# Performance work log

Measured on AMD Instinct MI355X. Metric: run time of the kernel, lower is better.

## Reference

```python
import jax, jax.numpy as jnp
import numpy as np

DIM = 768
NUM_HEADS = 12
HEAD_DIM = DIM // NUM_HEADS
SCALE = HEAD_DIM ** -0.5


def setup_inputs() -> dict:
    key = jax.random.key(0)
    ks = jax.random.split(key, 4)
    x = jax.random.normal(ks[0], (8, 1024, DIM), dtype=jnp.float32)
    # nn.Linear stores weight as [out, in]; we keep that convention.
    w_qkv = jax.random.normal(ks[1], (3 * DIM, DIM), dtype=jnp.float32) * (DIM ** -0.5)
    w_proj = jax.random.normal(ks[2], (DIM, DIM), dtype=jnp.float32) * (DIM ** -0.5)
    b_proj = jax.random.normal(ks[3], (DIM,), dtype=jnp.float32) * 0.02
    return {"x": x, "w_qkv": w_qkv, "w_proj": w_proj, "b_proj": b_proj}


def reference(x, w_qkv, w_proj, b_proj):
    B, N, C = x.shape
    H, D = NUM_HEADS, HEAD_DIM
    # qkv: [B, N, 3C] -> [3, B, H, N, D]
    qkv = jnp.einsum('bnc,oc->bno', x, w_qkv)
    qkv = qkv.reshape(B, N, 3, H, D).transpose(2, 0, 3, 1, 4)
    q, k, v = qkv[0] * SCALE, qkv[1], qkv[2]
    # attention scores [B, H, N, N]
    attn = jnp.einsum('bhnd,bhmd->bhnm', q, k)
    attn = jax.nn.softmax(attn, axis=-1)
    # weighted values -> [B, N, C]
    out = jnp.einsum('bhnm,bhmd->bhnd', attn, v)
    out = out.transpose(0, 2, 1, 3).reshape(B, N, C)
    # output projection
    return jnp.einsum('bnc,oc->bno', out, w_proj) + b_proj
```

## Files before the change

kernel.cpp:

```cpp
#include <hip/hip_runtime.h>
#include <hip/hip_bf16.h>
#include <math.h>


typedef unsigned short u16;
typedef __attribute__((ext_vector_type(8))) short bf16x8;
typedef __attribute__((ext_vector_type(4))) float f32x4;
typedef __attribute__((ext_vector_type(4))) unsigned int u32x4;

#define MFMA_BF16(a, b, c) __builtin_amdgcn_mfma_f32_16x16x32_bf16((a), (b), (c), 0, 0, 0)

static __device__ __forceinline__ void gld_lds16(const void* g, void* l) {
  __builtin_amdgcn_global_load_lds(
      (__attribute__((address_space(1))) void*)(g),
      (__attribute__((address_space(3))) void*)(l), 16, 0, 0);
}

static __device__ __forceinline__ u16 f2bf(float f) {
  __hip_bfloat16 h = __float2bfloat16(f);
  return *(u16*)&h;
}

static __device__ __forceinline__ float fast_exp2(float x) {
#if __has_builtin(__builtin_amdgcn_exp2f)
  return __builtin_amdgcn_exp2f(x);
#else
  return exp2f(x);
#endif
}

__global__ __launch_bounds__(256) void convert_kernel(
    const float* __restrict__ src, u16* __restrict__ dst, int n)
{
  const int i = (blockIdx.x * 256 + threadIdx.x) * 4;
  if (i + 3 >= n) {
    for (int k = 0; k < 4 && i + k < n; ++k) {
      float f = src[i + k];
      if (!isfinite(f)) f = 0.f;
      dst[i + k] = f2bf(f);
    }
    return;
  }
  const float4 v = *(const float4*)(src + i);
  float f0 = v.x, f1 = v.y, f2 = v.z, f3 = v.w;
  if (!isfinite(f0)) f0 = 0.f;
  if (!isfinite(f1)) f1 = 0.f;
  if (!isfinite(f2)) f2 = 0.f;
  if (!isfinite(f3)) f3 = 0.f;
  ushort4 o;
  o.x = f2bf(f0); o.y = f2bf(f1); o.z = f2bf(f2); o.w = f2bf(f3);
  *(ushort4*)(dst + i) = o;
}

__device__ __forceinline__ void gemm_tile_768(
    const u16* __restrict__ A, const u16* __restrict__ B,
    int m0, int n0, u16* ldsA, u16* ldsB, f32x4 acc[4][4])
{
  const int tid  = threadIdx.x;
  const int lane = tid & 63;
  const int wave = tid >> 6;
  const int quad = lane >> 4;
  const int l16  = lane & 15;
  const int wm = wave >> 1, wn = wave & 1;

  const u16* gA[4]; const u16* gB[4]; int ldsoff[4];
#pragma unroll
  for (int it = 0; it < 4; ++it) {
    const int c   = it * 256 + tid;
    const int row = c >> 3;
    const int cc  = (c & 7) ^ (row & 7);
    gA[it] = A + (size_t)(m0 + row) * 768 + cc * 8;
    gB[it] = B + (size_t)(n0 + row) * 768 + cc * 8;
    ldsoff[it] = (it * 256 + wave * 64) * 8;
  }

  for (int kt = 0; kt < 12; ++kt) {
    __syncthreads();
#pragma unroll
    for (int it = 0; it < 4; ++it) {
      gld_lds16(gA[it] + kt * 64, ldsA + ldsoff[it]);
      gld_lds16(gB[it] + kt * 64, ldsB + ldsoff[it]);
    }
    __syncthreads();
#pragma unroll
    for (int kc = 0; kc < 2; ++kc) {
      bf16x8 av[4], bv[4];
#pragma unroll
      for (int i = 0; i < 4; ++i) {
        const int rowA = wm * 64 + i * 16 + l16;
        av[i] = *(const bf16x8*)(ldsA + rowA * 64 + (((kc * 4 + quad) ^ (rowA & 7)) * 8));
        const int rowB = wn * 64 + i * 16 + l16;
        bv[i] = *(const bf16x8*)(ldsB + rowB * 64 + (((kc * 4 + quad) ^ (rowB & 7)) * 8));
      }
#pragma unroll
      for (int i = 0; i < 4; ++i)
#pragma unroll
        for (int j = 0; j < 4; ++j)
          acc[i][j] = MFMA_BF16(av[i], bv[j], acc[i][j]);
    }
  }
}


__global__ __launch_bounds__(256, 2) void qkv_gemm_kernel(
    const u16* __restrict__ X, const u16* __restrict__ W,
    __hip_bfloat16* __restrict__ Qb, __hip_bfloat16* __restrict__ Kb,
    __hip_bfloat16* __restrict__ Vb)
{
  __shared__ alignas(16) u16 ldsA[128 * 64];
  __shared__ alignas(16) u16 ldsB[128 * 64];
  const int n0 = blockIdx.x * 128;
  const int m0 = blockIdx.y * 128;
  f32x4 acc[4][4];
  const f32x4 zero = {0.f, 0.f, 0.f, 0.f};
#pragma unroll
  for (int i = 0; i < 4; ++i)
#pragma unroll
    for (int j = 0; j < 4; ++j) acc[i][j] = zero;

  gemm_tile_768(X, W, m0, n0, ldsA, ldsB, acc);

  const int tid = threadIdx.x, lane = tid & 63, wave = tid >> 6;
  const int quad = lane >> 4, l16 = lane & 15;
  const int wm = wave >> 1, wn = wave & 1;
#pragma unroll
  for (int j = 0; j < 4; ++j) {
    const int o = n0 + wn * 64 + j * 16 + l16;
    const int which = (o >= 1536) ? 2 : ((o >= 768) ? 1 : 0);
    const int oc = o - which * 768;
    const int h = oc >> 6, d = oc & 63;
    __hip_bfloat16* dst = (which == 0) ? Qb : ((which == 1) ? Kb : Vb);
    const float sc = (which == 0) ? 0.180336880f : 1.0f;
#pragma unroll
    for (int i = 0; i < 4; ++i) {
#pragma unroll
      for (int r = 0; r < 4; ++r) {
        const int m = m0 + wm * 64 + i * 16 + quad * 4 + r;
        const int b = m >> 10, n = m & 1023;
        const size_t idx = (((size_t)(b * 12 + h)) * 1024 + n) * 64 + d;
        dst[idx] = __float2bfloat16(acc[i][j][r] * sc);
      }
    }
  }
}

__global__ __launch_bounds__(256, 2) void proj_gemm_kernel(
    const u16* __restrict__ A, const u16* __restrict__ W,
    const float* __restrict__ bias, float* __restrict__ out)
{
  __shared__ alignas(16) u16 ldsA[128 * 64];
  __shared__ alignas(16) u16 ldsB[128 * 64];
  const int n0 = blockIdx.x * 128;
  const int m0 = blockIdx.y * 128;
  f32x4 acc[4][4];
  const f32x4 zero = {0.f, 0.f, 0.f, 0.f};
#pragma unroll
  for (int i = 0; i < 4; ++i)
#pragma unroll
    for (int j = 0; j < 4; ++j) acc[i][j] = zero;

  gemm_tile_768(A, W, m0, n0, ldsA, ldsB, acc);

  const int tid = threadIdx.x, lane = tid & 63, wave = tid >> 6;
  const int quad = lane >> 4, l16 = lane & 15;
  const int wm = wave >> 1, wn = wave & 1;
#pragma unroll
  for (int j = 0; j < 4; ++j) {
    const int o = n0 + wn * 64 + j * 16 + l16;
    const float bv = bias[o];
#pragma unroll
    for (int i = 0; i < 4; ++i)
#pragma unroll
      for (int r = 0; r < 4; ++r) {
        const int m = m0 + wm * 64 + i * 16 + quad * 4 + r;
        out[(size_t)m * 768 + o] = acc[i][j][r] + bv;
      }
  }
}

__global__ __launch_bounds__(256) void vtrans_kernel(
    const u16* __restrict__ V, u16* __restrict__ Vt)
{
  __shared__ alignas(16) u16 t[64][72];
  const int bh = blockIdx.x, nb = blockIdx.y;
  const int tid = threadIdx.x;
  const u16* src = V + ((size_t)bh * 1024 + nb * 64) * 64;
#pragma unroll
  for (int it = 0; it < 2; ++it) {
    const int c = it * 256 + tid;
    const int r = c >> 3, cc = c & 7;
    *(u32x4*)&t[r][cc * 8] = *(const u32x4*)(src + r * 64 + cc * 8);
  }
  __syncthreads();
  u16* dstbase = Vt + (size_t)bh * 64 * 1024 + nb * 64;
#pragma unroll
  for (int it = 0; it < 2; ++it) {
    const int c = it * 256 + tid;
    const int d = c >> 3, nc = c & 7;
    u32x4 o;
#pragma unroll
    for (int p = 0; p < 4; ++p) {
      const unsigned lo = t[nc * 8 + p * 2 + 0][d];
      const unsigned hi = t[nc * 8 + p * 2 + 1][d];
      o[p] = lo | (hi << 16);
    }
    *(u32x4*)(dstbase + (size_t)d * 1024 + nc * 8) = o;
  }
}

__global__ __launch_bounds__(256, 3) void attn_kernel(
    const u16* __restrict__ Q, const u16* __restrict__ K,
    const u16* __restrict__ Vt, __hip_bfloat16* __restrict__ O)
{
  __shared__ alignas(16) u16 ldsK[64 * 64];
  __shared__ alignas(16) u16 ldsV[64 * 64];
  __shared__ alignas(16) u16 pbuf[4 * 32 * 72];
  const int bh = blockIdx.x;
  const int qb = blockIdx.y;
  const int tid = threadIdx.x;
  const int wave = tid >> 6, lane = tid & 63;
  const int quad = lane >> 4, l16 = lane & 15;
  u16* pw = pbuf + wave * (32 * 72);

  const int q0 = qb * 128 + wave * 32;
  const u16* Kbh = K  + (size_t)bh * (1024 * 64);
  const u16* Vbh = Vt + (size_t)bh * (64 * 1024);

  const int c0   = tid;
  const int row0 = c0 >> 3,          slot0 = c0 & 7;
  const int row1 = (c0 + 256) >> 3,  slot1 = c0 & 7;
  const int cc0 = slot0 ^ (row0 & 7), cc1 = slot1 ^ (row1 & 7);
  const u16* gK0 = Kbh + (size_t)row0 * 64 + cc0 * 8;
  const u16* gK1 = Kbh + (size_t)row1 * 64 + cc1 * 8;
  const u16* gV0 = Vbh + (size_t)row0 * 1024 + cc0 * 8;
  const u16* gV1 = Vbh + (size_t)row1 * 1024 + cc1 * 8;
  const int ldso0 = (wave * 64) * 8, ldso1 = (256 + wave * 64) * 8;

  bf16x8 aQ0[2], aQ1[2];
#pragma unroll
  for (int s = 0; s < 2; ++s) {
    const u16* qp = Q + ((size_t)bh * 1024 + q0 + s * 16 + l16) * 64 + quad * 8;
    aQ0[s] = *(const bf16x8*)qp;
    aQ1[s] = *(const bf16x8*)(qp + 32);
  }

  f32x4 oacc[2][4];
  const f32x4 zero = {0.f, 0.f, 0.f, 0.f};
#pragma unroll
  for (int s = 0; s < 2; ++s)
#pragma unroll
    for (int db = 0; db < 4; ++db) oacc[s][db] = zero;
  float lacc[2][4] = {{0.f, 0.f, 0.f, 0.f}, {0.f, 0.f, 0.f, 0.f}};

  for (int kt = 0; kt < 16; ++kt) {
    __syncthreads();
    gld_lds16(gK0 + (size_t)kt * 64 * 64, ldsK + ldso0);
    gld_lds16(gK1 + (size_t)kt * 64 * 64, ldsK + ldso1);
    gld_lds16(gV0 + kt * 64, ldsV + ldso0);
    gld_lds16(gV1 + kt * 64, ldsV + ldso1);
    __syncthreads();

    bf16x8 kb0[4], kb1[4];
#pragma unroll
    for (int t = 0; t < 4; ++t) {
      const int row = t * 16 + l16;
      kb0[t] = *(const bf16x8*)(ldsK + row * 64 + (((0 * 4 + quad) ^ (row & 7)) * 8));
      kb1[t] = *(const bf16x8*)(ldsK + row * 64 + (((1 * 4 + quad) ^ (row & 7)) * 8));
    }
#pragma unroll
    for (int s = 0; s < 2; ++s) {
#pragma unroll
      for (int t = 0; t < 4; ++t) {
        f32x4 z = zero;
        z = MFMA_BF16(aQ0[s], kb0[t], z);
        z = MFMA_BF16(aQ1[s], kb1[t], z);
#pragma unroll
        for (int r = 0; r < 4; ++r) {
          const float p = fast_exp2(z[r]);
          lacc[s][r] += p;
          pw[(s * 16 + quad * 4 + r) * 72 + t * 16 + l16] = f2bf(p);
        }
      }
    }
    asm volatile("" ::: "memory");
    bf16x8 pa0[2], pa1[2];
#pragma unroll
    for (int s = 0; s < 2; ++s) {
      const u16* pb = pw + (s * 16 + l16) * 72 + quad * 8;
      pa0[s] = *(const bf16x8*)pb;
      pa1[s] = *(const bf16x8*)(pb + 32);
    }
#pragma unroll
    for (int db = 0; db < 4; ++db) {
      const int row = db * 16 + l16;
      const bf16x8 v0 = *(const bf16x8*)(ldsV + row * 64 + (((0 * 4 + quad) ^ (row & 7)) * 8));
      const bf16x8 v1 = *(const bf16x8*)(ldsV + row * 64 + (((1 * 4 + quad) ^ (row & 7)) * 8));
#pragma unroll
      for (int s = 0; s < 2; ++s) {
        oacc[s][db] = MFMA_BF16(pa0[s], v0, oacc[s][db]);
        oacc[s][db] = MFMA_BF16(pa1[s], v1, oacc[s][db]);
      }
    }
  }

  const int b = bh / 12, h = bh - (bh / 12) * 12;
#pragma unroll
  for (int s = 0; s < 2; ++s) {
#pragma unroll
    for (int r = 0; r < 4; ++r) {
      float lsum = lacc[s][r];
      lsum += __shfl_xor(lsum, 1);
      lsum += __shfl_xor(lsum, 2);
      lsum += __shfl_xor(lsum, 4);
      lsum += __shfl_xor(lsum, 8);
      const float inv = 1.f / lsum;
      const int n = q0 + s * 16 + quad * 4 + r;
      __hip_bfloat16* orow = O + ((size_t)b * 1024 + n) * 768 + h * 64;
#pragma unroll
      for (int db = 0; db < 4; ++db)
        orow[db * 16 + l16] = __float2bfloat16(oacc[s][db][r] * inv);
    }
  }
}

extern "C" void kernel_launch(void* const* d_in, const int* in_sizes, int n_in,
                              void* d_out, int out_size, void* d_ws, size_t ws_size,
                              hipStream_t stream) {
  const float* x      = (const float*)d_in[0];
  const float* w_qkv  = (const float*)d_in[1];
  const float* w_proj = (const float*)d_in[2];
  const float* b_proj = (const float*)d_in[3];
  float* out = (float*)d_out;

  char* ws = (char*)d_ws;
  const size_t SEG = (size_t)96 * 1024 * 64 * sizeof(u16);
  u16* xb   = (u16*)(ws + 0 * SEG);
  u16* Qb   = (u16*)(ws + 1 * SEG);
  u16* Kb   = (u16*)(ws + 2 * SEG);
  u16* Vb   = (u16*)(ws + 3 * SEG);
  u16* Vt   = (u16*)(ws + 4 * SEG);
  u16* wqb  = (u16*)(ws + 5 * SEG);
  u16* wpb  = (u16*)(ws + 5 * SEG + 3538944);
  u16* AO   = Vb;

  const int nx = 8 * 1024 * 768, nq = 2304 * 768, np = 768 * 768;
  convert_kernel<<<nx / 1024, 256, 0, stream>>>(x, xb, nx);
  convert_kernel<<<nq / 1024, 256, 0, stream>>>(w_qkv, wqb, nq);
  convert_kernel<<<np / 1024, 256, 0, stream>>>(w_proj, wpb, np);

  qkv_gemm_kernel<<<dim3(18, 64), 256, 0, stream>>>(
      xb, wqb, (__hip_bfloat16*)Qb, (__hip_bfloat16*)Kb, (__hip_bfloat16*)Vb);
  vtrans_kernel  <<<dim3(96, 16), 256, 0, stream>>>(Vb, Vt);
  attn_kernel    <<<dim3(96, 8), 256, 0, stream>>>(Qb, Kb, Vt, (__hip_bfloat16*)AO);
  proj_gemm_kernel<<<dim3(6, 64), 256, 0, stream>>>(AO, wpb, b_proj, out);
}
```

Measured before the change: 203.3 us.

## Fuse V transpose into QKV GEMM epilogue via LDS staging; merge weight conversions

The QKV GEMM epilogue now stages the output tile in LDS with a swizzled layout and writes Q/K rows and the transposed V directly using 16-byte vector stores. This removes the separate V-transpose kernel, its global round trip, and the scattered 2-byte stores of the old epilogue. The two weight conversions are also merged into one launch, and the scalar tail path in the converter is dropped. In exchange the epilogue adds two barriers and reuses the GEMM's shared memory.

Result: faster. 194.4 us (-4.4%).

```diff
diff --git a/kernel.cpp b/kernel.cpp
--- a/kernel.cpp
+++ b/kernel.cpp
@@ -29,18 +29,7 @@
 #endif
 }
 
-__global__ __launch_bounds__(256) void convert_kernel(
-    const float* __restrict__ src, u16* __restrict__ dst, int n)
-{
-  const int i = (blockIdx.x * 256 + threadIdx.x) * 4;
-  if (i + 3 >= n) {
-    for (int k = 0; k < 4 && i + k < n; ++k) {
-      float f = src[i + k];
-      if (!isfinite(f)) f = 0.f;
-      dst[i + k] = f2bf(f);
-    }
-    return;
-  }
+static __device__ __forceinline__ void conv4(const float* src, u16* dst, int i) {
   const float4 v = *(const float4*)(src + i);
   float f0 = v.x, f1 = v.y, f2 = v.z, f3 = v.w;
   if (!isfinite(f0)) f0 = 0.f;
@@ -52,6 +41,25 @@
   *(ushort4*)(dst + i) = o;
 }
 
+__global__ __launch_bounds__(256) void convert_kernel(
+    const float* __restrict__ src, u16* __restrict__ dst, int n)
+{
+  const int i = (blockIdx.x * 256 + threadIdx.x) * 4;
+  if (i < n) conv4(src, dst, i);
+}
+
+__global__ __launch_bounds__(256) void convert2_kernel(
+    const float* __restrict__ a, u16* __restrict__ da, int na_blk,
+    const float* __restrict__ b, u16* __restrict__ db)
+{
+  const int blk = blockIdx.x;
+  if (blk < na_blk) {
+    conv4(a, da, (blk * 256 + threadIdx.x) * 4);
+  } else {
+    conv4(b, db, ((blk - na_blk) * 256 + threadIdx.x) * 4);
+  }
+}
+
 __device__ __forceinline__ void gemm_tile_768(
     const u16* __restrict__ A, const u16* __restrict__ B,
     int m0, int n0, u16* ldsA, u16* ldsB, f32x4 acc[4][4])
@@ -104,8 +112,71 @@
 
 __global__ __launch_bounds__(256, 2) void qkv_gemm_kernel(
     const u16* __restrict__ X, const u16* __restrict__ W,
-    __hip_bfloat16* __restrict__ Qb, __hip_bfloat16* __restrict__ Kb,
-    __hip_bfloat16* __restrict__ Vb)
+    u16* __restrict__ Qb, u16* __restrict__ Kb, u16* __restrict__ Vt)
+{
+  __shared__ alignas(16) u16 lds[2 * 128 * 64];
+  u16* ldsA = lds;
+  u16* ldsB = lds + 128 * 64;
+  const int n0 = blockIdx.x * 128;
+  const int m0 = blockIdx.y * 128;
+  f32x4 acc[4][4];
+  const f32x4 zero = {0.f, 0.f, 0.f, 0.f};
+#pragma unroll
+  for (int i = 0; i < 4; ++i)
+#pragma unroll
+    for (int j = 0; j < 4; ++j) acc[i][j] = zero;
+
+  gemm_tile_768(X, W, m0, n0, ldsA, ldsB, acc);
+
+  const int tid = threadIdx.x, lane = tid & 63, wave = tid >> 6;
+  const int quad = lane >> 4, l16 = lane & 15;
+  const int wm = wave >> 1, wn = wave & 1;
+
+  const int which = blockIdx.x / 6;
+  const bool isV = (which == 2);
+  const float sc = (which == 0) ? 0.180336880f : 1.0f;
+  u16* ep = lds;
+
+  __syncthreads();
+#pragma unroll
+  for (int i = 0; i < 4; ++i)
+#pragma unroll
+    for (int j = 0; j < 4; ++j)
+#pragma unroll
+      for (int r = 0; r < 4; ++r) {
+        const int m_l = wm * 64 + i * 16 + quad * 4 + r;
+        const int o_l = wn * 64 + j * 16 + l16;
+        const int row = isV ? o_l : m_l;
+        const int col = isV ? m_l : o_l;
+        const int ch  = col >> 3;
+        const int chs = (ch & 8) | ((ch & 7) ^ (row & 7));
+        ep[row * 128 + chs * 8 + (col & 7)] = f2bf(acc[i][j][r] * sc);
+      }
+  __syncthreads();
+
+  const int row  = tid >> 1, half = tid & 1;
+  const int b_   = m0 >> 10;
+  const int nb   = m0 & 1023;
+  const int oc0  = n0 - which * 768;
+  u16* dst;
+  if (!isV) {
+    const int h = (oc0 >> 6) + half;
+    dst = (which == 0 ? Qb : Kb) + (((size_t)(b_ * 12 + h)) * 1024 + nb + row) * 64;
+  } else {
+    const int h = (oc0 >> 6) + (row >> 6);
+    const int d = row & 63;
+    dst = Vt + (((size_t)(b_ * 12 + h)) * 64 + d) * 1024 + nb + half * 64;
+  }
+#pragma unroll
+  for (int c = 0; c < 8; ++c) {
+    const int chs = half * 8 + (c ^ (row & 7));
+    *(u32x4*)(dst + c * 8) = *(const u32x4*)(ep + row * 128 + chs * 8);
+  }
+}
+
+__global__ __launch_bounds__(256, 2) void proj_gemm_kernel(
+    const u16* __restrict__ A, const u16* __restrict__ W,
+    const float* __restrict__ bias, float* __restrict__ out)
 {
   __shared__ alignas(16) u16 ldsA[128 * 64];
   __shared__ alignas(16) u16 ldsB[128 * 64];
@@ -118,7 +189,7 @@
 #pragma unroll
     for (int j = 0; j < 4; ++j) acc[i][j] = zero;
 
-  gemm_tile_768(X, W, m0, n0, ldsA, ldsB, acc);
+  gemm_tile_768(A, W, m0, n0, ldsA, ldsB, acc);
 
   const int tid = threadIdx.x, lane = tid & 63, wave = tid >> 6;
   const int quad = lane >> 4, l16 = lane & 15;
@@ -126,47 +197,6 @@
 #pragma unroll
   for (int j = 0; j < 4; ++j) {
     const int o = n0 + wn * 64 + j * 16 + l16;
-    const int which = (o >= 1536) ? 2 : ((o >= 768) ? 1 : 0);
-    const int oc = o - which * 768;
-    const int h = oc >> 6, d = oc & 63;
-    __hip_bfloat16* dst = (which == 0) ? Qb : ((which == 1) ? Kb : Vb);
-    const float sc = (which == 0) ? 0.180336880f : 1.0f;
-#pragma unroll
-    for (int i = 0; i < 4; ++i) {
-#pragma unroll
-      for (int r = 0; r < 4; ++r) {
-        const int m = m0 + wm * 64 + i * 16 + quad * 4 + r;
-        const int b = m >> 10, n = m & 1023;
-        const size_t idx = (((size_t)(b * 12 + h)) * 1024 + n) * 64 + d;
-        dst[idx] = __float2bfloat16(acc[i][j][r] * sc);
-      }
-    }
-  }
-}
-
-__global__ __launch_bounds__(256, 2) void proj_gemm_kernel(
-    const u16* __restrict__ A, const u16* __restrict__ W,
-    const float* __restrict__ bias, float* __restrict__ out)
-{
-  __shared__ alignas(16) u16 ldsA[128 * 64];
-  __shared__ alignas(16) u16 ldsB[128 * 64];
-  const int n0 = blockIdx.x * 128;
-  const int m0 = blockIdx.y * 128;
-  f32x4 acc[4][4];
-  const f32x4 zero = {0.f, 0.f, 0.f, 0.f};
-#pragma unroll
-  for (int i = 0; i < 4; ++i)
-#pragma unroll
-    for (int j = 0; j < 4; ++j) acc[i][j] = zero;
-
-  gemm_tile_768(A, W, m0, n0, ldsA, ldsB, acc);
-
-  const int tid = threadIdx.x, lane = tid & 63, wave = tid >> 6;
-  const int quad = lane >> 4, l16 = lane & 15;
-  const int wm = wave >> 1, wn = wave & 1;
-#pragma unroll
-  for (int j = 0; j < 4; ++j) {
-    const int o = n0 + wn * 64 + j * 16 + l16;
     const float bv = bias[o];
 #pragma unroll
     for (int i = 0; i < 4; ++i)
@@ -175,36 +205,6 @@
         const int m = m0 + wm * 64 + i * 16 + quad * 4 + r;
         out[(size_t)m * 768 + o] = acc[i][j][r] + bv;
       }
-  }
-}
-
-__global__ __launch_bounds__(256) void vtrans_kernel(
-    const u16* __restrict__ V, u16* __restrict__ Vt)
-{
-  __shared__ alignas(16) u16 t[64][72];
-  const int bh = blockIdx.x, nb = blockIdx.y;
-  const int tid = threadIdx.x;
-  const u16* src = V + ((size_t)bh * 1024 + nb * 64) * 64;
-#pragma unroll
-  for (int it = 0; it < 2; ++it) {
-    const int c = it * 256 + tid;
-    const int r = c >> 3, cc = c & 7;
-    *(u32x4*)&t[r][cc * 8] = *(const u32x4*)(src + r * 64 + cc * 8);
-  }
-  __syncthreads();
-  u16* dstbase = Vt + (size_t)bh * 64 * 1024 + nb * 64;
-#pragma unroll
-  for (int it = 0; it < 2; ++it) {
-    const int c = it * 256 + tid;
-    const int d = c >> 3, nc = c & 7;
-    u32x4 o;
-#pragma unroll
-    for (int p = 0; p < 4; ++p) {
-      const unsigned lo = t[nc * 8 + p * 2 + 0][d];
-      const unsigned hi = t[nc * 8 + p * 2 + 1][d];
-      o[p] = lo | (hi << 16);
-    }
-    *(u32x4*)(dstbase + (size_t)d * 1024 + nc * 8) = o;
   }
 }
 
@@ -337,20 +337,17 @@
   u16* xb   = (u16*)(ws + 0 * SEG);
   u16* Qb   = (u16*)(ws + 1 * SEG);
   u16* Kb   = (u16*)(ws + 2 * SEG);
-  u16* Vb   = (u16*)(ws + 3 * SEG);
+  u16* AO   = (u16*)(ws + 3 * SEG);
   u16* Vt   = (u16*)(ws + 4 * SEG);
   u16* wqb  = (u16*)(ws + 5 * SEG);
   u16* wpb  = (u16*)(ws + 5 * SEG + 3538944);
-  u16* AO   = Vb;
 
   const int nx = 8 * 1024 * 768, nq = 2304 * 768, np = 768 * 768;
-  convert_kernel<<<nx / 1024, 256, 0, stream>>>(x, xb, nx);
-  convert_kernel<<<nq / 1024, 256, 0, stream>>>(w_qkv, wqb, nq);
-  convert_kernel<<<np / 1024, 256, 0, stream>>>(w_proj, wpb, np);
-
-  qkv_gemm_kernel<<<dim3(18, 64), 256, 0, stream>>>(
-      xb, wqb, (__hip_bfloat16*)Qb, (__hip_bfloat16*)Kb, (__hip_bfloat16*)Vb);
-  vtrans_kernel  <<<dim3(96, 16), 256, 0, stream>>>(Vb, Vt);
+  convert_kernel <<<nx / 1024, 256, 0, stream>>>(x, xb, nx);
+  convert2_kernel<<<(nq + np) / 1024, 256, 0, stream>>>(w_qkv, wqb, nq / 1024,
+                                                        w_proj, wpb);
+
+  qkv_gemm_kernel<<<dim3(18, 64), 256, 0, stream>>>(xb, wqb, Qb, Kb, Vt);
   attn_kernel    <<<dim3(96, 8), 256, 0, stream>>>(Qb, Kb, Vt, (__hip_bfloat16*)AO);
   proj_gemm_kernel<<<dim3(6, 64), 256, 0, stream>>>(AO, wpb, b_proj, out);
 }
```
